# Optimization experiments

Measured on AMD Instinct MI355X. Metric: run time of the kernel, lower is better.

The kernel has to match this reference:

```python
import jax, jax.numpy as jnp
import numpy as np
from jax import lax

C = 512          # in_channels
L = 4            # fcos_conv_layers
NUM_CLS = 1      # fcos_num_class - 1
PRIOR_BIAS = float(-np.log((1 - 0.01) / 0.01))
BN_EPS = 1e-5


def conv1d(x, w, b, pad):
    # x: [B, Cin, T], w: [Cout, Cin, K]
    y = lax.conv_general_dilated(x, w, window_strides=(1,), padding=[(pad, pad)],
                                 dimension_numbers=('NCH', 'OIH', 'NCH'))
    return y + b[None, :, None]


def bn(x, g, b, m, v):
    inv = lax.rsqrt(v + BN_EPS)
    return (x - m[None, :, None]) * (g * inv)[None, :, None] + b[None, :, None]


def tower(x, ws, bs, gs, bes, ms, vs):
    # ws: [L, C, C, 3]; fixed small loop over layers
    for i in range(L):
        x = jax.nn.relu(bn(conv1d(x, ws[i], bs[i], 1), gs[i], bes[i], ms[i], vs[i]))
    return x


def setup_inputs() -> dict:
    key = jax.random.key(0)
    ks = jax.random.split(key, 32)
    d = {}
    d['f0'] = jax.random.normal(ks[0], (8, C, 1024), jnp.float32)
    d['f1'] = jax.random.normal(ks[1], (8, C, 512), jnp.float32)
    d['f2'] = jax.random.normal(ks[2], (8, C, 256), jnp.float32)

    def nrm(k, shape):
        return 0.01 * jax.random.normal(k, shape, jnp.float32)

    # cls / bbox towers: stacked conv + BN params
    d['cls_tw_w'] = nrm(ks[3], (L, C, C, 3)); d['cls_tw_b'] = jnp.zeros((L, C))
    d['cls_bn_g'] = jnp.ones((L, C)); d['cls_bn_b'] = jnp.zeros((L, C))
    d['cls_bn_m'] = jnp.zeros((L, C)); d['cls_bn_v'] = jnp.ones((L, C))
    d['box_tw_w'] = nrm(ks[4], (L, C, C, 3)); d['box_tw_b'] = jnp.zeros((L, C))
    d['box_bn_g'] = jnp.ones((L, C)); d['box_bn_b'] = jnp.zeros((L, C))
    d['box_bn_m'] = jnp.zeros((L, C)); d['box_bn_v'] = jnp.ones((L, C))

    d['logits_w'] = nrm(ks[5], (NUM_CLS, C, 3))
    d['logits_b'] = jnp.full((NUM_CLS,), PRIOR_BIAS, jnp.float32)
    d['bbox_w'] = nrm(ks[6], (2, C, 3)); d['bbox_b'] = jnp.zeros((2,))

    d['mix_w'] = nrm(ks[7], (C, 2 * C, 1)); d['mix_b'] = jnp.zeros((C,))
    d['mix_bn_g'] = jnp.ones((C,)); d['mix_bn_b'] = jnp.zeros((C,))
    d['mix_bn_m'] = jnp.zeros((C,)); d['mix_bn_v'] = jnp.ones((C,))

    d['iou_w1'] = nrm(ks[8], (C // 2, C, 3)); d['iou_b1'] = jnp.zeros((C // 2,))
    d['iou_bn_g'] = jnp.ones((C // 2,)); d['iou_bn_b'] = jnp.zeros((C // 2,))
    d['iou_bn_m'] = jnp.zeros((C // 2,)); d['iou_bn_v'] = jnp.ones((C // 2,))
    d['iou_w2'] = nrm(ks[9], (1, C // 2, 1)); d['iou_b2'] = jnp.zeros((1,))

    d['scales'] = jnp.ones((3,), jnp.float32)
    return d


def reference(f0, f1, f2,
              cls_tw_w, cls_tw_b, cls_bn_g, cls_bn_b, cls_bn_m, cls_bn_v,
              box_tw_w, box_tw_b, box_bn_g, box_bn_b, box_bn_m, box_bn_v,
              logits_w, logits_b, bbox_w, bbox_b,
              mix_w, mix_b, mix_bn_g, mix_bn_b, mix_bn_m, mix_bn_v,
              iou_w1, iou_b1, iou_bn_g, iou_bn_b, iou_bn_m, iou_bn_v,
              iou_w2, iou_b2, scales):
    outs = []
    for l, x in enumerate([f0, f1, f2]):
        ct = tower(x, cls_tw_w, cls_tw_b, cls_bn_g, cls_bn_b, cls_bn_m, cls_bn_v)
        bt = tower(x, box_tw_w, box_tw_b, box_bn_g, box_bn_b, box_bn_m, box_bn_v)
        logits = conv1d(ct, logits_w, logits_b, 1)                      # [B, 1, T]
        bbox = jnp.exp(conv1d(bt, bbox_w, bbox_b, 1) * scales[l])       # [B, 2, T]
        mix = jax.nn.relu(bn(conv1d(jnp.concatenate([ct, bt], axis=1), mix_w, mix_b, 0),
                             mix_bn_g, mix_bn_b, mix_bn_m, mix_bn_v))   # [B, C, T]
        h = jax.nn.relu(bn(conv1d(mix, iou_w1, iou_b1, 1),
                           iou_bn_g, iou_bn_b, iou_bn_m, iou_bn_v))
        iou = conv1d(h, iou_w2, iou_b2, 0)                              # [B, 1, T]
        outs.append(jnp.concatenate([logits, bbox, iou], axis=1))       # [B, 4, T]
    return jnp.concatenate(outs, axis=-1)  # [B, 4, T0+T1+T2]
```

## Files before the change

### kernel.cpp

```cpp
#include <hip/hip_runtime.h>
#include <hip/hip_bf16.h>


typedef __bf16 bf16x8 __attribute__((ext_vector_type(8)));
typedef float f32x4 __attribute__((ext_vector_type(4)));

__device__ __forceinline__ float bf2f(unsigned short u) {
    union { unsigned int i; float f; } c; c.i = ((unsigned int)u) << 16; return c.f;
}
__device__ __forceinline__ unsigned short f2bf(float f) {
    union { __hip_bfloat16 h; unsigned short u; } c; c.h = __float2bfloat16(f); return c.u;
}

__device__ __forceinline__ void gload16(const void* g, void* l) {
    __builtin_amdgcn_global_load_lds(
        (const __attribute__((address_space(1))) unsigned int*)g,
        (__attribute__((address_space(3))) unsigned int*)l,
        16, 0, 0);
}

__device__ __forceinline__ void tile_decode(int ct, int& rowstart, int& t0, int& Tl) {
    if (ct < 64)      { Tl = 1024; int b = ct >> 3;              t0 = (ct & 7) << 7; rowstart = b * 1024; }
    else if (ct < 96) { Tl = 512;  int i = ct - 64; int b = i >> 2; t0 = (i & 3) << 7; rowstart = 8192 + b * 512; }
    else              { Tl = 256;  int i = ct - 96; int b = i >> 1; t0 = (i & 1) << 7; rowstart = 12288 + b * 256; }
}

template<int KSIZE>
__global__ __launch_bounds__(256)
void conv_gemm(const unsigned short* __restrict__ X, int xstride, int ci0_base, int ci_twstride, int Cin,
               const unsigned short* __restrict__ W, int w_twstride,
               const float* __restrict__ Bs, int b_twstride,
               unsigned short* __restrict__ Y, int ystride, int co_twstride,
               int relu)
{
    constexpr int BM = 128, BN = 128, BK = 32;
    constexpr int NR = BN + KSIZE - 1;
    constexpr int XSEG = (NR * 64 + 1023) / 1024;
    constexpr int WSEG = KSIZE * BM * 64 / 1024;
    constexpr int WPW  = WSEG / 4;
    __shared__ alignas(16) unsigned short Xs[XSEG * 512];
    __shared__ alignas(16) unsigned short Ws[WSEG * 512];

    const int tid = threadIdx.x;
    const int lane = tid & 63, wid = tid >> 6;
    int rowstart, t0, Tl;
    tile_decode(blockIdx.x, rowstart, t0, Tl);
    const int co0 = blockIdx.y * BM;
    const int tw = blockIdx.z;
    const int ci_off = ci0_base + tw * ci_twstride;
    const unsigned short* Wp = W + (size_t)tw * w_twstride;
    const float* Bp = Bs + tw * b_twstride;
    const int co_out0 = tw * co_twstride + co0;

    const int wm = (wid >> 1) * 64, wn = (wid & 1) * 64;
    const int lr = lane & 15;
    const int sr = lane >> 4;

    const unsigned short* xga[3]; bool xval[3]; unsigned short* xl[3];
#pragma unroll
    for (int p = 0; p < 3; ++p) {
        int seg = p * 4 + wid;
        xval[p] = false; xga[p] = X; xl[p] = Xs;
        if (seg < XSEG) {
            xl[p] = Xs + seg * 512;
            int g = seg * 64 + lane;
            int row = g >> 2, s = (g & 3) ^ ((row >> 1) & 3);
            int t = t0 + row - (KSIZE >> 1);
            if (row < NR && t >= 0 && t < Tl) {
                xval[p] = true;
                xga[p] = X + (size_t)(rowstart + t) * xstride + ci_off + s * 8;
            }
        }
    }
    const unsigned short* wga[WPW]; unsigned short* wl[WPW];
#pragma unroll
    for (int p = 0; p < WPW; ++p) {
        int seg = p * 4 + wid;
        wl[p] = Ws + seg * 512;
        int g = seg * 64 + lane;
        int row = g >> 2, s = (g & 3) ^ ((row >> 1) & 3);
        int co = row & (BM - 1), kk = row >> 7;
        wga[p] = Wp + (size_t)(co0 + co) * (KSIZE * Cin) + kk * Cin + s * 8;
    }

#pragma unroll
    for (int p = 0; p < 3; ++p) {
        int seg = p * 4 + wid;
        if (seg < XSEG && !xval[p])
            *(uint4*)(xl[p] + lane * 8) = make_uint4(0u, 0u, 0u, 0u);
    }

    f32x4 acc[4][4];
#pragma unroll
    for (int i = 0; i < 4; ++i)
#pragma unroll
        for (int j = 0; j < 4; ++j) acc[i][j] = (f32x4){0.f, 0.f, 0.f, 0.f};

    const int nk = Cin / BK;
    for (int ks = 0; ks < nk; ++ks) {
#pragma unroll
        for (int p = 0; p < 3; ++p)
            if (xval[p]) gload16(xga[p], xl[p]);
#pragma unroll
        for (int p = 0; p < WPW; ++p) gload16(wga[p], wl[p]);
#pragma unroll
        for (int p = 0; p < 3; ++p) xga[p] += BK;
#pragma unroll
        for (int p = 0; p < WPW; ++p) wga[p] += BK;
        __syncthreads();

#pragma unroll
        for (int kk = 0; kk < KSIZE; ++kk) {
            bf16x8 af[4], bv[4];
#pragma unroll
            for (int mi = 0; mi < 4; ++mi) {
                int ra = kk * BM + wm + mi * 16 + lr;
                af[mi] = *(const bf16x8*)((const char*)Ws + ra * 64 + (((sr ^ (ra >> 1)) & 3) << 4));
                int rb = wn + mi * 16 + lr + kk;
                bv[mi] = *(const bf16x8*)((const char*)Xs + rb * 64 + (((sr ^ (rb >> 1)) & 3) << 4));
            }
#pragma unroll
            for (int mi = 0; mi < 4; ++mi)
#pragma unroll
                for (int ni = 0; ni < 4; ++ni)
                    acc[mi][ni] = __builtin_amdgcn_mfma_f32_16x16x32_bf16(af[mi], bv[ni], acc[mi][ni], 0, 0, 0);
        }
        __syncthreads();
    }

    const int r4 = (lane >> 4) * 4;
#pragma unroll
    for (int mi = 0; mi < 4; ++mi) {
        int co_l = wm + mi * 16 + r4;
        float b0 = Bp[co0 + co_l + 0], b1 = Bp[co0 + co_l + 1];
        float b2 = Bp[co0 + co_l + 2], b3 = Bp[co0 + co_l + 3];
#pragma unroll
        for (int ni = 0; ni < 4; ++ni) {
            int t = t0 + wn + ni * 16 + lr;
            f32x4 a = acc[mi][ni];
            float v0 = a[0] + b0, v1 = a[1] + b1, v2 = a[2] + b2, v3 = a[3] + b3;
            if (relu) {
                v0 = fmaxf(v0, 0.f); v1 = fmaxf(v1, 0.f);
                v2 = fmaxf(v2, 0.f); v3 = fmaxf(v3, 0.f);
            }
            union { unsigned long long u; unsigned short s[4]; } pk;
            pk.s[0] = f2bf(v0); pk.s[1] = f2bf(v1); pk.s[2] = f2bf(v2); pk.s[3] = f2bf(v3);
            *(unsigned long long*)(Y + (size_t)(rowstart + t) * ystride + co_out0 + co_l) = pk.u;
        }
    }
}

__global__ __launch_bounds__(256)
void transpose_in(const float* __restrict__ f0, const float* __restrict__ f1, const float* __restrict__ f2,
                  unsigned short* __restrict__ act0)
{
    __shared__ float tile[32][33];
    int bx = blockIdx.x;
    const float* src; int Tl, roff, b, t0;
    if (bx < 256)      { src = f0; Tl = 1024; roff = 0;     int i = bx;       b = i >> 5; t0 = (i & 31) << 5; }
    else if (bx < 384) { src = f1; Tl = 512;  roff = 8192;  int i = bx - 256; b = i >> 4; t0 = (i & 15) << 5; }
    else               { src = f2; Tl = 256;  roff = 12288; int i = bx - 384; b = i >> 3; t0 = (i & 7)  << 5; }
    int c0 = blockIdx.y << 5;
    const float* sb = src + (size_t)b * 512 * Tl;
    int tl = threadIdx.x & 31, cl = threadIdx.x >> 5;
#pragma unroll
    for (int j = 0; j < 4; ++j) {
        int c = cl + j * 8;
        tile[c][tl] = sb[(size_t)(c0 + c) * Tl + t0 + tl];
    }
    __syncthreads();
    int cc = threadIdx.x & 31, tr0 = threadIdx.x >> 5;
    size_t base = (size_t)(roff + b * Tl + t0) * 512 + c0;
#pragma unroll
    for (int j = 0; j < 4; ++j) {
        int tr = tr0 + j * 8;
        act0[base + (size_t)tr * 512 + cc] = f2bf(tile[cc][tr]);
    }
}

__global__ __launch_bounds__(256)
void prep_tower(const float* __restrict__ cls_w, const float* __restrict__ box_w,
                const float* __restrict__ cg, const float* __restrict__ cvv,
                const float* __restrict__ bg, const float* __restrict__ bvv,
                unsigned short* __restrict__ Wt)
{
    int idx = blockIdx.x * 256 + threadIdx.x;
    if (idx >= 2 * 4 * 512 * 3 * 512) return;
    int ci = idx & 511;
    int kk = (idx >> 9) % 3;
    int co = (idx / 1536) & 511;
    int l  = (idx / 786432) & 3;
    int tw = idx / 3145728;
    const float* w = tw ? box_w : cls_w;
    const float* g = tw ? bg : cg;
    const float* v = tw ? bvv : cvv;
    float s = g[l * 512 + co] * rsqrtf(v[l * 512 + co] + 1e-5f);
    float val = w[(((size_t)(l * 512 + co)) * 512 + ci) * 3 + kk] * s;
    Wt[idx] = f2bf(val);
}

__global__ __launch_bounds__(256)
void prep_misc(const float* mix_w, const float* mix_b, const float* mg, const float* mbeta, const float* mm, const float* mv,
               const float* iou_w1, const float* iou_b1, const float* ig, const float* ibeta, const float* im, const float* iv,
               const float* cls_b, const float* cg, const float* cbeta, const float* cm, const float* cv2,
               const float* box_b, const float* bg, const float* bbeta, const float* bm, const float* bv2,
               unsigned short* Wmix, unsigned short* Wiou, float* Bt, float* Bmix, float* Biou)
{
    int idx = blockIdx.x * 256 + threadIdx.x;
    if (idx < 524288) {
        int co = idx >> 10;
        float s = mg[co] * rsqrtf(mv[co] + 1e-5f);
        Wmix[idx] = f2bf(mix_w[idx] * s);
        return;
    }
    idx -= 524288;
    if (idx < 393216) {
        int ci = idx & 511, kk = (idx >> 9) % 3, co = idx / 1536;
        float s = ig[co] * rsqrtf(iv[co] + 1e-5f);
        Wiou[idx] = f2bf(iou_w1[((size_t)(co * 512 + ci)) * 3 + kk] * s);
        return;
    }
    idx -= 393216;
    if (idx < 4096) {
        int co = idx & 511, l = (idx >> 9) & 3, tw = idx >> 11;
        const float* g = tw ? bg : cg; const float* v = tw ? bv2 : cv2;
        const float* m = tw ? bm : cm; const float* be = tw ? bbeta : cbeta;
        const float* cb = tw ? box_b : cls_b;
        int o = l * 512 + co;
        float s = g[o] * rsqrtf(v[o] + 1e-5f);
        Bt[idx] = (cb[o] - m[o]) * s + be[o];
        return;
    }
    idx -= 4096;
    if (idx < 512) {
        float s = mg[idx] * rsqrtf(mv[idx] + 1e-5f);
        Bmix[idx] = (mix_b[idx] - mm[idx]) * s + mbeta[idx];
        return;
    }
    idx -= 512;
    if (idx < 256) {
        float s = ig[idx] * rsqrtf(iv[idx] + 1e-5f);
        Biou[idx] = (iou_b1[idx] - im[idx]) * s + ibeta[idx];
    }
}

__global__ __launch_bounds__(256)
void heads_kernel(const unsigned short* __restrict__ catb, const unsigned short* __restrict__ iouh,
                  const float* __restrict__ lw, const float* __restrict__ lb,
                  const float* __restrict__ bw, const float* __restrict__ bb,
                  const float* __restrict__ iw, const float* __restrict__ ib,
                  const float* __restrict__ scales, float* __restrict__ out)
{
    const int lane = threadIdx.x & 63;
    const int wid = threadIdx.x >> 6;

    float lwr[24], bwr0[24], bwr1[24], iwr[4];
    {
        const float4* p = (const float4*)(lw + lane * 24);
#pragma unroll
        for (int q = 0; q < 6; ++q) {
            float4 v = p[q];
            lwr[q * 4 + 0] = v.x; lwr[q * 4 + 1] = v.y; lwr[q * 4 + 2] = v.z; lwr[q * 4 + 3] = v.w;
        }
        p = (const float4*)(bw + lane * 24);
#pragma unroll
        for (int q = 0; q < 6; ++q) {
            float4 v = p[q];
            bwr0[q * 4 + 0] = v.x; bwr0[q * 4 + 1] = v.y; bwr0[q * 4 + 2] = v.z; bwr0[q * 4 + 3] = v.w;
        }
        p = (const float4*)(bw + 1536 + lane * 24);
#pragma unroll
        for (int q = 0; q < 6; ++q) {
            float4 v = p[q];
            bwr1[q * 4 + 0] = v.x; bwr1[q * 4 + 1] = v.y; bwr1[q * 4 + 2] = v.z; bwr1[q * 4 + 3] = v.w;
        }
        float4 v = *(const float4*)(iw + lane * 4);
        iwr[0] = v.x; iwr[1] = v.y; iwr[2] = v.z; iwr[3] = v.w;
    }
    const float lb0 = lb[0], bb0 = bb[0], bb1 = bb[1], ib0 = ib[0];
    const float s0 = scales[0], s1 = scales[1], s2 = scales[2];

    for (int r = blockIdx.x * 4 + wid; r < 14336; r += gridDim.x * 4) {
        int tlog, roff, tgoff; float sc;
        if (r < 8192)       { tlog = 10; roff = 0;     tgoff = 0;    sc = s0; }
        else if (r < 12288) { tlog = 9;  roff = 8192;  tgoff = 1024; sc = s1; }
        else                { tlog = 8;  roff = 12288; tgoff = 1536; sc = s2; }
        int i = r - roff;
        int Tl = 1 << tlog;
        int b = i >> tlog, t = i & (Tl - 1);

        float al = 0.f, a0 = 0.f, a1 = 0.f, ai = 0.f;
        const unsigned short* base = catb + (size_t)r * 1024 + lane * 8;
#pragma unroll
        for (int kk = 0; kk < 3; ++kk) {
            int tt = t + kk - 1;
            if (tt < 0 || tt >= Tl) continue;
            union { uint4 u; unsigned short s[8]; } cv, bv;
            cv.u = *(const uint4*)(base + (kk - 1) * 1024);
            bv.u = *(const uint4*)(base + (kk - 1) * 1024 + 512);
#pragma unroll
            for (int j = 0; j < 8; ++j) {
                float xc = bf2f(cv.s[j]);
                float xb = bf2f(bv.s[j]);
                al = fmaf(xc, lwr[j * 3 + kk], al);
                a0 = fmaf(xb, bwr0[j * 3 + kk], a0);
                a1 = fmaf(xb, bwr1[j * 3 + kk], a1);
            }
        }
        {
            union { uint2 u; unsigned short s[4]; } hv;
            hv.u = *(const uint2*)(iouh + (size_t)r * 256 + lane * 4);
#pragma unroll
            for (int j = 0; j < 4; ++j) ai = fmaf(bf2f(hv.s[j]), iwr[j], ai);
        }
#pragma unroll
        for (int off = 32; off > 0; off >>= 1) {
            al += __shfl_xor(al, off);
            a0 += __shfl_xor(a0, off);
            a1 += __shfl_xor(a1, off);
            ai += __shfl_xor(ai, off);
        }
        if (lane == 0) {
            int tg = tgoff + t;
            out[((size_t)b * 4 + 0) * 1792 + tg] = al + lb0;
            out[((size_t)b * 4 + 1) * 1792 + tg] = expf((a0 + bb0) * sc);
            out[((size_t)b * 4 + 2) * 1792 + tg] = expf((a1 + bb1) * sc);
            out[((size_t)b * 4 + 3) * 1792 + tg] = ai + ib0;
        }
    }
}

extern "C" void kernel_launch(void* const* d_in, const int* in_sizes, int n_in,
                              void* d_out, int out_size, void* d_ws, size_t ws_size,
                              hipStream_t stream)
{
    const float* f0       = (const float*)d_in[0];
    const float* f1       = (const float*)d_in[1];
    const float* f2       = (const float*)d_in[2];
    const float* cls_tw_w = (const float*)d_in[3];
    const float* cls_tw_b = (const float*)d_in[4];
    const float* cls_bn_g = (const float*)d_in[5];
    const float* cls_bn_b = (const float*)d_in[6];
    const float* cls_bn_m = (const float*)d_in[7];
    const float* cls_bn_v = (const float*)d_in[8];
    const float* box_tw_w = (const float*)d_in[9];
    const float* box_tw_b = (const float*)d_in[10];
    const float* box_bn_g = (const float*)d_in[11];
    const float* box_bn_b = (const float*)d_in[12];
    const float* box_bn_m = (const float*)d_in[13];
    const float* box_bn_v = (const float*)d_in[14];
    const float* logits_w = (const float*)d_in[15];
    const float* logits_b = (const float*)d_in[16];
    const float* bbox_w   = (const float*)d_in[17];
    const float* bbox_b   = (const float*)d_in[18];
    const float* mix_w    = (const float*)d_in[19];
    const float* mix_b    = (const float*)d_in[20];
    const float* mix_bn_g = (const float*)d_in[21];
    const float* mix_bn_b = (const float*)d_in[22];
    const float* mix_bn_m = (const float*)d_in[23];
    const float* mix_bn_v = (const float*)d_in[24];
    const float* iou_w1   = (const float*)d_in[25];
    const float* iou_b1   = (const float*)d_in[26];
    const float* iou_bn_g = (const float*)d_in[27];
    const float* iou_bn_b = (const float*)d_in[28];
    const float* iou_bn_m = (const float*)d_in[29];
    const float* iou_bn_v = (const float*)d_in[30];
    const float* iou_w2   = (const float*)d_in[31];
    const float* iou_b2   = (const float*)d_in[32];
    const float* scales   = (const float*)d_in[33];

    unsigned char* ws = (unsigned char*)d_ws;
    unsigned short* Wt   = (unsigned short*)(ws + 0);
    unsigned short* Wmix = (unsigned short*)(ws + 12582912);
    unsigned short* Wiou = (unsigned short*)(ws + 13631488);
    float*          Bt   = (float*)(ws + 14417920);
    float*          Bmix = (float*)(ws + 14434304);
    float*          Biou = (float*)(ws + 14436352);
    unsigned short* act0 = (unsigned short*)(ws + 14437376);
    unsigned short* catA = (unsigned short*)(ws + 29117440);
    unsigned short* catB = (unsigned short*)(ws + 58477568);
    unsigned short* mixo = (unsigned short*)(ws + 87837696);
    unsigned short* iouh = (unsigned short*)(ws + 102517760);

    prep_tower<<<dim3(24576), dim3(256), 0, stream>>>(cls_tw_w, box_tw_w, cls_bn_g, cls_bn_v,
                                                      box_bn_g, box_bn_v, Wt);
    prep_misc<<<dim3(3603), dim3(256), 0, stream>>>(mix_w, mix_b, mix_bn_g, mix_bn_b, mix_bn_m, mix_bn_v,
                                                    iou_w1, iou_b1, iou_bn_g, iou_bn_b, iou_bn_m, iou_bn_v,
                                                    cls_tw_b, cls_bn_g, cls_bn_b, cls_bn_m, cls_bn_v,
                                                    box_tw_b, box_bn_g, box_bn_b, box_bn_m, box_bn_v,
                                                    Wmix, Wiou, Bt, Bmix, Biou);
    transpose_in<<<dim3(448, 16), dim3(256), 0, stream>>>(f0, f1, f2, act0);

    conv_gemm<3><<<dim3(112, 4, 2), 256, 0, stream>>>(act0, 512, 0, 0, 512,
                                                      Wt, 3145728, Bt, 2048, catA, 1024, 512, 1);
    conv_gemm<3><<<dim3(112, 4, 2), 256, 0, stream>>>(catA, 1024, 0, 512, 512,
                                                      Wt + 786432, 3145728, Bt + 512, 2048, catB, 1024, 512, 1);
    conv_gemm<3><<<dim3(112, 4, 2), 256, 0, stream>>>(catB, 1024, 0, 512, 512,
                                                      Wt + 1572864, 3145728, Bt + 1024, 2048, catA, 1024, 512, 1);
    conv_gemm<3><<<dim3(112, 4, 2), 256, 0, stream>>>(catA, 1024, 0, 512, 512,
                                                      Wt + 2359296, 3145728, Bt + 1536, 2048, catB, 1024, 512, 1);
    conv_gemm<1><<<dim3(112, 4, 1), 256, 0, stream>>>(catB, 1024, 0, 0, 1024,
                                                      Wmix, 0, Bmix, 0, mixo, 512, 0, 1);
    conv_gemm<3><<<dim3(112, 2, 1), 256, 0, stream>>>(mixo, 512, 0, 0, 512,
                                                      Wiou, 0, Biou, 0, iouh, 256, 0, 1);
    heads_kernel<<<dim3(896), dim3(256), 0, stream>>>(catB, iouh, logits_w, logits_b,
                                                      bbox_w, bbox_b, iou_w2, iou_b2, scales,
                                                      (float*)d_out);
}
```

Measured before the change: 323.4 us.

## Pad activation rows with zero halos and double-buffer conv GEMM LDS loads

```diff
diff --git a/kernel.cpp b/kernel.cpp
--- a/kernel.cpp
+++ b/kernel.cpp
@@ -20,9 +20,9 @@
 }
 
 __device__ __forceinline__ void tile_decode(int ct, int& rowstart, int& t0, int& Tl) {
-    if (ct < 64)      { Tl = 1024; int b = ct >> 3;              t0 = (ct & 7) << 7; rowstart = b * 1024; }
-    else if (ct < 96) { Tl = 512;  int i = ct - 64; int b = i >> 2; t0 = (i & 3) << 7; rowstart = 8192 + b * 512; }
-    else              { Tl = 256;  int i = ct - 96; int b = i >> 1; t0 = (i & 1) << 7; rowstart = 12288 + b * 256; }
+    if (ct < 64)      { Tl = 1024; int b = ct >> 3;                 t0 = (ct & 7) << 7; rowstart = b * 1026 + 1; }
+    else if (ct < 96) { Tl = 512;  int i = ct - 64; int b = i >> 2; t0 = (i & 3) << 7; rowstart = 8208 + b * 514 + 1; }
+    else              { Tl = 256;  int i = ct - 96; int b = i >> 1; t0 = (i & 1) << 7; rowstart = 12320 + b * 258 + 1; }
 }
 
 template<int KSIZE>
@@ -36,10 +36,11 @@
     constexpr int BM = 128, BN = 128, BK = 32;
     constexpr int NR = BN + KSIZE - 1;
     constexpr int XSEG = (NR * 64 + 1023) / 1024;
+    constexpr int XPW  = (XSEG + 3) / 4;
     constexpr int WSEG = KSIZE * BM * 64 / 1024;
     constexpr int WPW  = WSEG / 4;
-    __shared__ alignas(16) unsigned short Xs[XSEG * 512];
-    __shared__ alignas(16) unsigned short Ws[WSEG * 512];
+    __shared__ alignas(16) unsigned short Xs[2 * XSEG * 512];
+    __shared__ alignas(16) unsigned short Ws[2 * WSEG * 512];
 
     const int tid = threadIdx.x;
     const int lane = tid & 63, wid = tid >> 6;
@@ -56,21 +57,14 @@
     const int lr = lane & 15;
     const int sr = lane >> 4;
 
-    const unsigned short* xga[3]; bool xval[3]; unsigned short* xl[3];
-#pragma unroll
-    for (int p = 0; p < 3; ++p) {
-        int seg = p * 4 + wid;
-        xval[p] = false; xga[p] = X; xl[p] = Xs;
-        if (seg < XSEG) {
-            xl[p] = Xs + seg * 512;
-            int g = seg * 64 + lane;
-            int row = g >> 2, s = (g & 3) ^ ((row >> 1) & 3);
-            int t = t0 + row - (KSIZE >> 1);
-            if (row < NR && t >= 0 && t < Tl) {
-                xval[p] = true;
-                xga[p] = X + (size_t)(rowstart + t) * xstride + ci_off + s * 8;
-            }
-        }
+    const unsigned short* xga[XPW]; unsigned short* xl[XPW];
+#pragma unroll
+    for (int p = 0; p < XPW; ++p) {
+        int seg = (KSIZE == 3) ? ((p < 2) ? p * 4 + wid : 8) : (p * 4 + wid);
+        xl[p] = Xs + seg * 512;
+        int g = seg * 64 + lane;
+        int row = g >> 2, s = (g & 3) ^ ((row >> 1) & 3);
+        xga[p] = X + (size_t)(rowstart - (KSIZE >> 1) + row) * xstride + ci_off + s * 8;
     }
     const unsigned short* wga[WPW]; unsigned short* wl[WPW];
 #pragma unroll
@@ -83,41 +77,44 @@
         wga[p] = Wp + (size_t)(co0 + co) * (KSIZE * Cin) + kk * Cin + s * 8;
     }
 
-#pragma unroll
-    for (int p = 0; p < 3; ++p) {
-        int seg = p * 4 + wid;
-        if (seg < XSEG && !xval[p])
-            *(uint4*)(xl[p] + lane * 8) = make_uint4(0u, 0u, 0u, 0u);
-    }
-
     f32x4 acc[4][4];
 #pragma unroll
     for (int i = 0; i < 4; ++i)
 #pragma unroll
         for (int j = 0; j < 4; ++j) acc[i][j] = (f32x4){0.f, 0.f, 0.f, 0.f};
 
+    auto STAGE = [&](int buf) {
+#pragma unroll
+        for (int p = 0; p < XPW; ++p) { gload16(xga[p], xl[p] + buf * (XSEG * 512)); xga[p] += BK; }
+#pragma unroll
+        for (int p = 0; p < WPW; ++p) { gload16(wga[p], wl[p] + buf * (WSEG * 512)); wga[p] += BK; }
+    };
+
     const int nk = Cin / BK;
+    STAGE(0);
+    int cur = 0;
     for (int ks = 0; ks < nk; ++ks) {
-#pragma unroll
-        for (int p = 0; p < 3; ++p)
-            if (xval[p]) gload16(xga[p], xl[p]);
-#pragma unroll
-        for (int p = 0; p < WPW; ++p) gload16(wga[p], wl[p]);
-#pragma unroll
-        for (int p = 0; p < 3; ++p) xga[p] += BK;
-#pragma unroll
-        for (int p = 0; p < WPW; ++p) wga[p] += BK;
-        __syncthreads();
-
+        if (ks + 1 < nk) {
+            STAGE(cur ^ 1);
+            if constexpr (KSIZE == 3) asm volatile("s_waitcnt vmcnt(9)" ::: "memory");
+            else                      asm volatile("s_waitcnt vmcnt(4)" ::: "memory");
+        } else {
+            asm volatile("s_waitcnt vmcnt(0)" ::: "memory");
+        }
+        __builtin_amdgcn_sched_barrier(0);
+        __builtin_amdgcn_s_barrier();
+
+        const char* bXs = (const char*)Xs + cur * (XSEG * 1024);
+        const char* bWs = (const char*)Ws + cur * (WSEG * 1024);
 #pragma unroll
         for (int kk = 0; kk < KSIZE; ++kk) {
             bf16x8 af[4], bv[4];
 #pragma unroll
             for (int mi = 0; mi < 4; ++mi) {
                 int ra = kk * BM + wm + mi * 16 + lr;
-                af[mi] = *(const bf16x8*)((const char*)Ws + ra * 64 + (((sr ^ (ra >> 1)) & 3) << 4));
+                af[mi] = *(const bf16x8*)(bWs + ra * 64 + (((sr ^ (ra >> 1)) & 3) << 4));
                 int rb = wn + mi * 16 + lr + kk;
-                bv[mi] = *(const bf16x8*)((const char*)Xs + rb * 64 + (((sr ^ (rb >> 1)) & 3) << 4));
+                bv[mi] = *(const bf16x8*)(bXs + rb * 64 + (((sr ^ (rb >> 1)) & 3) << 4));
             }
 #pragma unroll
             for (int mi = 0; mi < 4; ++mi)
@@ -125,7 +122,9 @@
                 for (int ni = 0; ni < 4; ++ni)
                     acc[mi][ni] = __builtin_amdgcn_mfma_f32_16x16x32_bf16(af[mi], bv[ni], acc[mi][ni], 0, 0, 0);
         }
-        __syncthreads();
+        __builtin_amdgcn_sched_barrier(0);
+        __builtin_amdgcn_s_barrier();
+        cur ^= 1;
     }
 
     const int r4 = (lane >> 4) * 4;
@@ -151,15 +150,35 @@
 }
 
 __global__ __launch_bounds__(256)
+void zero_pads(unsigned short* __restrict__ act0, unsigned short* __restrict__ catA,
+               unsigned short* __restrict__ catB, unsigned short* __restrict__ mixo,
+               unsigned short* __restrict__ iouh)
+{
+    int c = blockIdx.x >> 1, side = blockIdx.x & 1;
+    int start, Tl;
+    if (c < 8)       { start = c * 1026;               Tl = 1024; }
+    else if (c < 16) { start = 8208 + (c - 8) * 514;   Tl = 512;  }
+    else             { start = 12320 + (c - 16) * 258; Tl = 256;  }
+    size_t prow = start + (side ? Tl + 1 : 0);
+    int tid = threadIdx.x;
+    uint4 z = make_uint4(0u, 0u, 0u, 0u);
+    if (tid < 64)  *(uint4*)(act0 + prow * 512 + tid * 8) = z;
+    if (tid < 128) { *(uint4*)(catA + prow * 1024 + tid * 8) = z;
+                     *(uint4*)(catB + prow * 1024 + tid * 8) = z; }
+    if (tid >= 128 && tid < 192) *(uint4*)(mixo + prow * 512 + (tid - 128) * 8) = z;
+    if (tid >= 192 && tid < 224) *(uint4*)(iouh + prow * 256 + (tid - 192) * 8) = z;
+}
+
+__global__ __launch_bounds__(256)
 void transpose_in(const float* __restrict__ f0, const float* __restrict__ f1, const float* __restrict__ f2,
                   unsigned short* __restrict__ act0)
 {
     __shared__ float tile[32][33];
     int bx = blockIdx.x;
-    const float* src; int Tl, roff, b, t0;
-    if (bx < 256)      { src = f0; Tl = 1024; roff = 0;     int i = bx;       b = i >> 5; t0 = (i & 31) << 5; }
-    else if (bx < 384) { src = f1; Tl = 512;  roff = 8192;  int i = bx - 256; b = i >> 4; t0 = (i & 15) << 5; }
-    else               { src = f2; Tl = 256;  roff = 12288; int i = bx - 384; b = i >> 3; t0 = (i & 7)  << 5; }
+    const float* src; int Tl, padbase, b, t0;
+    if (bx < 256)      { src = f0; Tl = 1024; int i = bx;       b = i >> 5; t0 = (i & 31) << 5; padbase = b * 1026; }
+    else if (bx < 384) { src = f1; Tl = 512;  int i = bx - 256; b = i >> 4; t0 = (i & 15) << 5; padbase = 8208 + b * 514; }
+    else               { src = f2; Tl = 256;  int i = bx - 384; b = i >> 3; t0 = (i & 7)  << 5; padbase = 12320 + b * 258; }
     int c0 = blockIdx.y << 5;
     const float* sb = src + (size_t)b * 512 * Tl;
     int tl = threadIdx.x & 31, cl = threadIdx.x >> 5;
@@ -170,7 +189,7 @@
     }
     __syncthreads();
     int cc = threadIdx.x & 31, tr0 = threadIdx.x >> 5;
-    size_t base = (size_t)(roff + b * Tl + t0) * 512 + c0;
+    size_t base = (size_t)(padbase + 1 + t0) * 512 + c0;
 #pragma unroll
     for (int j = 0; j < 4; ++j) {
         int tr = tr0 + j * 8;
@@ -281,20 +300,22 @@
     const float s0 = scales[0], s1 = scales[1], s2 = scales[2];
 
     for (int r = blockIdx.x * 4 + wid; r < 14336; r += gridDim.x * 4) {
-        int tlog, roff, tgoff; float sc;
+        int tlog, roff, tgoff, padbase; float sc;
         if (r < 8192)       { tlog = 10; roff = 0;     tgoff = 0;    sc = s0; }
         else if (r < 12288) { tlog = 9;  roff = 8192;  tgoff = 1024; sc = s1; }
         else                { tlog = 8;  roff = 12288; tgoff = 1536; sc = s2; }
         int i = r - roff;
         int Tl = 1 << tlog;
         int b = i >> tlog, t = i & (Tl - 1);
+        if (r < 8192)       padbase = b * 1026;
+        else if (r < 12288) padbase = 8208 + b * 514;
+        else                padbase = 12320 + b * 258;
+        int prow = padbase + 1 + t;
 
         float al = 0.f, a0 = 0.f, a1 = 0.f, ai = 0.f;
-        const unsigned short* base = catb + (size_t)r * 1024 + lane * 8;
+        const unsigned short* base = catb + (size_t)prow * 1024 + lane * 8;
 #pragma unroll
         for (int kk = 0; kk < 3; ++kk) {
-            int tt = t + kk - 1;
-            if (tt < 0 || tt >= Tl) continue;
             union { uint4 u; unsigned short s[8]; } cv, bv;
             cv.u = *(const uint4*)(base + (kk - 1) * 1024);
             bv.u = *(const uint4*)(base + (kk - 1) * 1024 + 512);
@@ -309,7 +330,7 @@
         }
         {
             union { uint2 u; unsigned short s[4]; } hv;
-            hv.u = *(const uint2*)(iouh + (size_t)r * 256 + lane * 4);
+            hv.u = *(const uint2*)(iouh + (size_t)prow * 256 + lane * 4);
 #pragma unroll
             for (int j = 0; j < 4; ++j) ai = fmaf(bf2f(hv.s[j]), iwr[j], ai);
         }
@@ -377,11 +398,12 @@
     float*          Bmix = (float*)(ws + 14434304);
     float*          Biou = (float*)(ws + 14436352);
     unsigned short* act0 = (unsigned short*)(ws + 14437376);
-    unsigned short* catA = (unsigned short*)(ws + 29117440);
-    unsigned short* catB = (unsigned short*)(ws + 58477568);
-    unsigned short* mixo = (unsigned short*)(ws + 87837696);
-    unsigned short* iouh = (unsigned short*)(ws + 102517760);
-
+    unsigned short* catA = (unsigned short*)(ws + 29182976);
+    unsigned short* catB = (unsigned short*)(ws + 58674176);
+    unsigned short* mixo = (unsigned short*)(ws + 88165376);
+    unsigned short* iouh = (unsigned short*)(ws + 102910976);
+
+    zero_pads<<<dim3(48), dim3(256), 0, stream>>>(act0, catA, catB, mixo, iouh);
     prep_tower<<<dim3(24576), dim3(256), 0, stream>>>(cls_tw_w, box_tw_w, cls_bn_g, cls_bn_v,
                                                       box_bn_g, box_bn_v, Wt);
     prep_misc<<<dim3(3603), dim3(256), 0, stream>>>(mix_w, mix_b, mix_bn_g, mix_bn_b, mix_bn_m, mix_bn_v,
```

Result: no change. 317.2 us (-1.9%).
